# Performance work log

Measured on AMD Instinct MI355X. Metric: run time of the kernel, lower is better.

The kernel has to match this reference:

```python
import jax, jax.numpy as jnp
import numpy as np

B, N, D = 4, 1024, 512
H, Dv, Dq = 8, 64, 64
NUM_BUCKETS = 64
LN_EPS = 1e-5


def setup_inputs() -> dict:
    key = jax.random.key(0)
    ks = jax.random.split(key, 10)
    x = jax.random.normal(ks[0], (B, N, D), dtype=jnp.float32)
    ts = jnp.sort(jax.random.randint(ks[1], (B, N), 0, 1_000_000), axis=1).astype(jnp.int64)
    cm = jnp.triu(jnp.ones((N, N), dtype=bool), k=1)  # causal: mask j > i
    pm = jnp.zeros((B, N), dtype=bool)                # no padding
    uvqk = 0.02 * jax.random.normal(ks[2], (D, 2 * H * Dv + 2 * H * Dq), dtype=jnp.float32)
    lim = float(np.sqrt(6.0 / (H * Dv + D)))
    o_w = jax.random.uniform(ks[3], (H * Dv, D), minval=-lim, maxval=lim, dtype=jnp.float32)
    o_b = jnp.zeros((D,), dtype=jnp.float32)
    ln_x_w = jnp.ones((D,), jnp.float32); ln_x_b = jnp.zeros((D,), jnp.float32)
    ln_a_w = jnp.ones((H * Dv,), jnp.float32); ln_a_b = jnp.zeros((H * Dv,), jnp.float32)
    ts_w = 0.02 * jax.random.normal(ks[4], (NUM_BUCKETS + 1,), dtype=jnp.float32)
    pos_w = 0.02 * jax.random.normal(ks[5], (2 * N - 1,), dtype=jnp.float32)
    return {"x": x, "ts": ts, "cm": cm, "pm": pm, "uvqk": uvqk, "o_w": o_w, "o_b": o_b,
            "ln_x_w": ln_x_w, "ln_x_b": ln_x_b, "ln_a_w": ln_a_w, "ln_a_b": ln_a_b,
            "ts_w": ts_w, "pos_w": pos_w}


def _layernorm(x, w, b):
    m = jnp.mean(x, axis=-1, keepdims=True)
    v = jnp.mean(jnp.square(x - m), axis=-1, keepdims=True)
    return (x - m) / jnp.sqrt(v + LN_EPS) * w + b


def _rel_bias(ts, ts_w, pos_w):
    # positional part: pb[i, j] = pos_w[j - i + N - 1], shape [N, N]
    idx = jnp.arange(N)
    pb = pos_w[idx[None, :] - idx[:, None] + N - 1]
    # bucketed time part
    ext = jnp.concatenate([ts, ts[:, N - 1:N]], axis=1)           # [B, N+1]
    diff = ext[:, 1:, None] - ext[:, None, :-1]                   # [B, N, N]
    logd = jnp.log(jnp.maximum(jnp.abs(diff), 1).astype(jnp.float32))
    bk = jnp.clip((logd / 0.301).astype(jnp.int32), 0, NUM_BUCKETS)
    return pb[None] + ts_w[bk]                                    # [B, N, N]


def reference(x, ts, cm, pm, uvqk, o_w, o_b, ln_x_w, ln_x_b, ln_a_w, ln_a_b, ts_w, pos_w):
    nx = _layernorm(x, ln_x_w, ln_x_b)                            # [B, N, D]
    out = jax.nn.silu(jnp.einsum('bnd,de->bne', nx, uvqk))        # [B, N, 2HDv+2HDq]
    u, v, q, k = jnp.split(out, [H * Dv, 2 * H * Dv, 2 * H * Dv + H * Dq], axis=-1)
    q = q.reshape(B, N, H, Dq)
    k = k.reshape(B, N, H, Dq)
    v = v.reshape(B, N, H, Dv)
    qk = jnp.einsum('bihd,bjhd->bhij', q, k) + _rel_bias(ts, ts_w, pos_w)[:, None]
    qk = jax.nn.silu(qk) / N
    qk = jnp.where(cm[None, None], 0.0, qk)          # causal mask
    qk = jnp.where(pm[:, None, None, :], 0.0, qk)    # padding mask on keys
    ao = jnp.einsum('bhij,bjhd->bihd', qk, v).reshape(B, N, H * Dv)
    ao = _layernorm(ao, ln_a_w, ln_a_b)
    u = u.reshape(B, N, H * Dv)
    y = (u * ao) @ o_w + o_b + x
    return jnp.where(pm[:, :, None], 0.0, y)
```

## Files before the change

kernel.cpp:

```cpp
#include <hip/hip_runtime.h>
#include <hip/hip_bf16.h>


typedef __attribute__((ext_vector_type(8))) short short8;
typedef __attribute__((ext_vector_type(4))) short bf4;
typedef __attribute__((ext_vector_type(4))) float floatx4;

#define MFMA_BF16 __builtin_amdgcn_mfma_f32_16x16x32_bf16

static __device__ __forceinline__ short f2bf(float f) {
  unsigned u = __builtin_bit_cast(unsigned, f);
  u = (u + 0x7fffu + ((u >> 16) & 1u)) >> 16;
  return (short)u;
}
static __device__ __forceinline__ unsigned pk_bf16(float a, float b) {
  __hip_bfloat162 h = __float22bfloat162_rn(float2{a, b});
  unsigned u;
  __builtin_memcpy(&u, &h, 4);
  return u;
}
static __device__ __forceinline__ short lo16(unsigned u) { return (short)(u & 0xffffu); }
static __device__ __forceinline__ short hi16(unsigned u) { return (short)(u >> 16); }
static __device__ __forceinline__ float bf2f(short s) {
  unsigned u = ((unsigned)(unsigned short)s) << 16;
  return __builtin_bit_cast(float, u);
}
static __device__ __forceinline__ float silu_f(float x) {
  return x / (1.f + __expf(-x));
}
static __device__ __forceinline__ void gl_lds16(const void* g, void* l) {
  __builtin_amdgcn_global_load_lds(
      (const __attribute__((address_space(1))) unsigned int*)g,
      (__attribute__((address_space(3))) unsigned int*)l, 16, 0, 0);
}

__global__ __launch_bounds__(256) void prep_kernel(
    const float* __restrict__ x, const int* __restrict__ ts,
    const float* __restrict__ uvqk, const float* __restrict__ o_w,
    const float* __restrict__ ln_x_w, const float* __restrict__ ln_x_b,
    const float* __restrict__ ts_w, const float* __restrict__ pos_w,
    short* __restrict__ nx, short* __restrict__ uvqk_t,
    short* __restrict__ o_wt, short* __restrict__ bias) {
  __shared__ float tile[32][33];
  const int id = blockIdx.x;
  const int t = threadIdx.x;
  if (id < 4096) {
    const int b = id >> 10, i = id & 1023;
    int ie = i + 1; if (ie > 1023) ie = 1023;
    const int tse = ts[(b << 10) + ie];
    const int j0 = t * 4;
    int4 tj = *(const int4*)&ts[(b << 10) + j0];
    const int* tjp = (const int*)&tj;
    float ov[4];
#pragma unroll
    for (int e = 0; e < 4; ++e) {
      int dt = tse - tjp[e];
      float ad = fabsf((float)dt);
      if (ad < 1.f) ad = 1.f;
      int bkt = (int)(__logf(ad) * (1.f / 0.301f));
      if (bkt > 64) bkt = 64;
      ov[e] = pos_w[j0 + e - i + 1023] + ts_w[bkt];
    }
    uint2 o2 = {pk_bf16(ov[0], ov[1]), pk_bf16(ov[2], ov[3])};
    *(uint2*)&bias[((size_t)id << 10) + j0] = o2;
  } else if (id < 5120) {
    const int lane = t & 63;
    const int row = ((id - 4096) << 2) + (t >> 6);
    const int c0 = lane * 8;
    const float* xr = x + (size_t)row * 512;
    float v[8];
    *(float4*)&v[0] = *(const float4*)(xr + c0);
    *(float4*)&v[4] = *(const float4*)(xr + c0 + 4);
    float s = 0.f, sq = 0.f;
#pragma unroll
    for (int e = 0; e < 8; ++e) { s += v[e]; sq += v[e] * v[e]; }
#pragma unroll
    for (int off = 32; off > 0; off >>= 1) {
      s += __shfl_xor(s, off);
      sq += __shfl_xor(sq, off);
    }
    float m = s * (1.f / 512.f);
    float var = sq * (1.f / 512.f) - m * m;
    float rinv = rsqrtf(var + 1e-5f);
    float wv[8], bv[8];
    *(float4*)&wv[0] = *(const float4*)(ln_x_w + c0);
    *(float4*)&wv[4] = *(const float4*)(ln_x_w + c0 + 4);
    *(float4*)&bv[0] = *(const float4*)(ln_x_b + c0);
    *(float4*)&bv[4] = *(const float4*)(ln_x_b + c0 + 4);
    float o[8];
#pragma unroll
    for (int e = 0; e < 8; ++e) o[e] = (v[e] - m) * rinv * wv[e] + bv[e];
    uint4 o4 = {pk_bf16(o[0], o[1]), pk_bf16(o[2], o[3]),
                pk_bf16(o[4], o[5]), pk_bf16(o[6], o[7])};
    *(uint4*)(nx + (size_t)row * 512 + c0) = o4;
  } else {
    const float* src; short* dst; int R, C, bc, br;
    if (id < 6144) {
      int idm = id - 5120;
      src = uvqk; dst = uvqk_t; R = 512; C = 2048;
      bc = (idm & 63) * 32; br = (idm >> 6) * 32;
    } else {
      int idm = id - 6144;
      src = o_w; dst = o_wt; R = 512; C = 512;
      bc = (idm & 15) * 32; br = (idm >> 4) * 32;
    }
    const int c = t & 31, r0 = t >> 5;
#pragma unroll
    for (int p = 0; p < 4; ++p) {
      int r = r0 + p * 8;
      tile[r][c] = src[(size_t)(br + r) * C + bc + c];
    }
    __syncthreads();
#pragma unroll
    for (int p = 0; p < 4; ++p) {
      int r = r0 + p * 8;
      dst[(size_t)(bc + r) * R + br + c] = f2bf(tile[c][r]);
    }
  }
}

__global__ __launch_bounds__(256) void gemm1_kernel(
    const short* __restrict__ A, const short* __restrict__ Bt,
    short* __restrict__ u_buf, short* __restrict__ vt_buf,
    short* __restrict__ q_buf, short* __restrict__ k_buf) {
  __shared__ __align__(16) short As[2][128 * 32];
  __shared__ __align__(16) short Bs[2][128 * 32];
  const int t = threadIdx.x;
  const int lane = t & 63, w = t >> 6;
  const int quad = lane >> 4, l15 = lane & 15;
  const int m0 = blockIdx.x * 128, n0 = blockIdx.y * 128;
  const int wm = (w & 1) * 64, wn = (w >> 1) * 64;
  const int lr = lane >> 2, lc = (lane & 3) * 8;
  floatx4 acc[4][4];
#pragma unroll
  for (int i = 0; i < 4; ++i)
#pragma unroll
    for (int j = 0; j < 4; ++j) acc[i][j] = (floatx4){0.f, 0.f, 0.f, 0.f};

  for (int k0 = 0; k0 < 512; k0 += 64) {
    __syncthreads();
#pragma unroll
    for (int c = 0; c < 2; ++c)
#pragma unroll
      for (int p = 0; p < 2; ++p) {
        int ra = w * 32 + p * 16;
        gl_lds16(&A[(size_t)(m0 + ra + lr) * 512 + k0 + c * 32 + lc], &As[c][ra * 32]);
        gl_lds16(&Bt[(size_t)(n0 + ra + lr) * 512 + k0 + c * 32 + lc], &Bs[c][ra * 32]);
      }
    __syncthreads();
#pragma unroll
    for (int c = 0; c < 2; ++c) {
      short8 af[4], bfr[4];
#pragma unroll
      for (int mi = 0; mi < 4; ++mi) af[mi] = *(const short8*)&As[c][(wm + mi * 16 + l15) * 32 + quad * 8];
#pragma unroll
      for (int ni = 0; ni < 4; ++ni) bfr[ni] = *(const short8*)&Bs[c][(wn + ni * 16 + l15) * 32 + quad * 8];
#pragma unroll
      for (int mi = 0; mi < 4; ++mi)
#pragma unroll
        for (int ni = 0; ni < 4; ++ni)
          acc[mi][ni] = MFMA_BF16(af[mi], bfr[ni], acc[mi][ni], 0, 0, 0);
    }
  }
  const int seg = n0 >> 9, cbase = n0 & 511;
  if (seg == 0) {
#pragma unroll
    for (int mi = 0; mi < 4; ++mi)
#pragma unroll
      for (int ni = 0; ni < 4; ++ni) {
        int row0 = m0 + wm + mi * 16 + quad * 4;
        int c = cbase + wn + ni * 16 + l15;
        float v0 = silu_f(acc[mi][ni][0]), v1 = silu_f(acc[mi][ni][1]);
        float v2 = silu_f(acc[mi][ni][2]), v3 = silu_f(acc[mi][ni][3]);
        unsigned pa = pk_bf16(v0, v1), pb = pk_bf16(v2, v3);
        u_buf[(size_t)row0 * 512 + c] = lo16(pa);
        u_buf[(size_t)(row0 + 1) * 512 + c] = hi16(pa);
        u_buf[(size_t)(row0 + 2) * 512 + c] = lo16(pb);
        u_buf[(size_t)(row0 + 3) * 512 + c] = hi16(pb);
      }
  } else if (seg == 1) {
#pragma unroll
    for (int mi = 0; mi < 4; ++mi)
#pragma unroll
      for (int ni = 0; ni < 4; ++ni) {
        int c = cbase + wn + ni * 16 + l15;
        int h = c >> 6, d = c & 63;
        int row0 = m0 + wm + mi * 16 + quad * 4;
        int b_ = row0 >> 10, nb = row0 & 1023;
        float v0 = silu_f(acc[mi][ni][0]) * (1.f / 1024.f);
        float v1 = silu_f(acc[mi][ni][1]) * (1.f / 1024.f);
        float v2 = silu_f(acc[mi][ni][2]) * (1.f / 1024.f);
        float v3 = silu_f(acc[mi][ni][3]) * (1.f / 1024.f);
        uint2 sv = {pk_bf16(v0, v1), pk_bf16(v2, v3)};
        *(uint2*)&vt_buf[(((size_t)(b_ * 8 + h) * 64 + d) << 10) + nb] = sv;
      }
  } else {
    short* dst = (seg == 2) ? q_buf : k_buf;
#pragma unroll
    for (int mi = 0; mi < 4; ++mi)
#pragma unroll
      for (int ni = 0; ni < 4; ++ni) {
        int row0 = m0 + wm + mi * 16 + quad * 4;
        int c = cbase + wn + ni * 16 + l15;
        int b_ = row0 >> 10, nb = row0 & 1023;
        size_t base = ((((size_t)(b_ * 8 + (c >> 6))) << 10) + nb) * 64 + (c & 63);
        float v0 = silu_f(acc[mi][ni][0]), v1 = silu_f(acc[mi][ni][1]);
        float v2 = silu_f(acc[mi][ni][2]), v3 = silu_f(acc[mi][ni][3]);
        unsigned pa = pk_bf16(v0, v1), pb = pk_bf16(v2, v3);
        dst[base] = lo16(pa);
        dst[base + 64] = hi16(pa);
        dst[base + 128] = lo16(pb);
        dst[base + 192] = hi16(pb);
      }
  }
}

__global__ __launch_bounds__(256, 4) void attn_kernel(
    const short* __restrict__ q_buf, const short* __restrict__ k_buf,
    const short* __restrict__ vt_buf, const short* __restrict__ bias_buf,
    short* __restrict__ ao_part) {
  __shared__ __align__(16) short q_s[64][72];
  __shared__ __align__(16) short k_s[64][72];
  __shared__ __align__(16) short vt_s[64][72];
  __shared__ __align__(16) short p_s[64][72];

  const int t = threadIdx.x;
  const int lane = t & 63, w = t >> 6;
  const int quad = lane >> 4, l15 = lane & 15;
  const int bh = blockIdx.x, pair = blockIdx.y, jh = blockIdx.z;
  const int b = bh >> 3, h = bh & 7;
  const short* qh = q_buf + (size_t)bh * 65536;
  const short* kh = k_buf + (size_t)bh * 65536;
  const short* vth = vt_buf + (size_t)bh * 65536;
  const int sr = t >> 2, sc = (t & 3) * 16;

#pragma unroll
  for (int half = 0; half < 2; ++half) {
    const int it = half ? (15 - pair) : pair;
    const int i0 = it * 64;
    {
      float4 qr0 = *(const float4*)&qh[(size_t)(i0 + sr) * 64 + sc];
      float4 qr1 = *(const float4*)&qh[(size_t)(i0 + sr) * 64 + sc + 8];
      *(float4*)&q_s[sr][sc] = qr0;
      *(float4*)&q_s[sr][sc + 8] = qr1;
    }
    float4 kr0, kr1, vr0, vr1;
    if (jh <= it) {
      int j0 = jh * 64;
      kr0 = *(const float4*)&kh[(size_t)(j0 + sr) * 64 + sc];
      kr1 = *(const float4*)&kh[(size_t)(j0 + sr) * 64 + sc + 8];
      vr0 = *(const float4*)&vth[(size_t)sr * 1024 + j0 + sc];
      vr1 = *(const float4*)&vth[(size_t)sr * 1024 + j0 + sc + 8];
    }
    floatx4 ao0 = {0.f, 0.f, 0.f, 0.f}, ao1 = ao0, ao2 = ao0, ao3 = ao0;
    for (int jt = jh; jt <= it; jt += 4) {
      const int j0 = jt * 64;
      short br[4][4];
      {
        const short* bb = &bias_buf[((size_t)(b * 1024 + i0 + w * 16 + quad * 4) << 10) + j0 + l15];
#pragma unroll
        for (int ni = 0; ni < 4; ++ni)
#pragma unroll
          for (int r2 = 0; r2 < 4; ++r2)
            br[ni][r2] = bb[((size_t)r2 << 10) + ni * 16];
      }
      __syncthreads();
      *(float4*)&k_s[sr][sc] = kr0;
      *(float4*)&k_s[sr][sc + 8] = kr1;
      *(float4*)&vt_s[sr][sc] = vr0;
      *(float4*)&vt_s[sr][sc + 8] = vr1;
      {
        int jn = (jt + 4 <= it) ? jt + 4 : jt;
        int jn0 = jn * 64;
        kr0 = *(const float4*)&kh[(size_t)(jn0 + sr) * 64 + sc];
        kr1 = *(const float4*)&kh[(size_t)(jn0 + sr) * 64 + sc + 8];
        vr0 = *(const float4*)&vth[(size_t)sr * 1024 + jn0 + sc];
        vr1 = *(const float4*)&vth[(size_t)sr * 1024 + jn0 + sc + 8];
      }
      __syncthreads();
      floatx4 s0, s1, s2, s3;
#pragma unroll
      for (int r2 = 0; r2 < 4; ++r2) {
        s0[r2] = bf2f(br[0][r2]);
        s1[r2] = bf2f(br[1][r2]);
        s2[r2] = bf2f(br[2][r2]);
        s3[r2] = bf2f(br[3][r2]);
      }
#pragma unroll
      for (int kk = 0; kk < 64; kk += 32) {
        short8 aq = *(const short8*)&q_s[w * 16 + l15][kk + quad * 8];
        s0 = MFMA_BF16(aq, *(const short8*)&k_s[0 + l15][kk + quad * 8], s0, 0, 0, 0);
        s1 = MFMA_BF16(aq, *(const short8*)&k_s[16 + l15][kk + quad * 8], s1, 0, 0, 0);
        s2 = MFMA_BF16(aq, *(const short8*)&k_s[32 + l15][kk + quad * 8], s2, 0, 0, 0);
        s3 = MFMA_BF16(aq, *(const short8*)&k_s[48 + l15][kk + quad * 8], s3, 0, 0, 0);
      }
      const bool diag = (jt == it);
      floatx4 sv[4] = {s0, s1, s2, s3};
#pragma unroll
      for (int ni = 0; ni < 4; ++ni) {
        int j_loc = ni * 16 + l15;
        float pv[4];
#pragma unroll
        for (int r2 = 0; r2 < 4; ++r2) {
          int i_loc = w * 16 + quad * 4 + r2;
          float p = silu_f(sv[ni][r2]);
          pv[r2] = (diag && j_loc > i_loc) ? 0.f : p;
        }
        unsigned pa = pk_bf16(pv[0], pv[1]), pb = pk_bf16(pv[2], pv[3]);
        int ib = w * 16 + quad * 4;
        p_s[ib][j_loc] = lo16(pa);
        p_s[ib + 1][j_loc] = hi16(pa);
        p_s[ib + 2][j_loc] = lo16(pb);
        p_s[ib + 3][j_loc] = hi16(pb);
      }
#pragma unroll
      for (int kk = 0; kk < 64; kk += 32) {
        short8 ap = *(const short8*)&p_s[w * 16 + l15][kk + quad * 8];
        ao0 = MFMA_BF16(ap, *(const short8*)&vt_s[0 + l15][kk + quad * 8], ao0, 0, 0, 0);
        ao1 = MFMA_BF16(ap, *(const short8*)&vt_s[16 + l15][kk + quad * 8], ao1, 0, 0, 0);
        ao2 = MFMA_BF16(ap, *(const short8*)&vt_s[32 + l15][kk + quad * 8], ao2, 0, 0, 0);
        ao3 = MFMA_BF16(ap, *(const short8*)&vt_s[48 + l15][kk + quad * 8], ao3, 0, 0, 0);
      }
    }
    floatx4 aov[4] = {ao0, ao1, ao2, ao3};
    short* aod = ao_part + (size_t)jh * 2097152;
#pragma unroll
    for (int ni = 0; ni < 4; ++ni) {
      int gi0 = i0 + w * 16 + quad * 4;
      int d = ni * 16 + l15;
      unsigned pa = pk_bf16(aov[ni][0], aov[ni][1]);
      unsigned pb = pk_bf16(aov[ni][2], aov[ni][3]);
      size_t base = ((size_t)(b * 1024 + gi0)) * 512 + h * 64 + d;
      aod[base] = lo16(pa);
      aod[base + 512] = hi16(pa);
      aod[base + 1024] = lo16(pb);
      aod[base + 1536] = hi16(pb);
    }
  }
}

__global__ __launch_bounds__(256) void ln_mul_kernel(
    const short* __restrict__ ao_part, const short* __restrict__ u,
    const float* __restrict__ w_, const float* __restrict__ b_,
    short* __restrict__ g) {
  const int lane = threadIdx.x & 63;
  const int row = (blockIdx.x << 2) + (threadIdx.x >> 6);
  const int c0 = lane * 8;
  short8 a0 = *(const short8*)(ao_part + (size_t)row * 512 + c0);
  short8 a1 = *(const short8*)(ao_part + 2097152 + (size_t)row * 512 + c0);
  short8 a2 = *(const short8*)(ao_part + 4194304 + (size_t)row * 512 + c0);
  short8 a3 = *(const short8*)(ao_part + 6291456 + (size_t)row * 512 + c0);
  float v[8];
#pragma unroll
  for (int e = 0; e < 8; ++e)
    v[e] = (bf2f(a0[e]) + bf2f(a1[e])) + (bf2f(a2[e]) + bf2f(a3[e]));
  float s = 0.f, sq = 0.f;
#pragma unroll
  for (int e = 0; e < 8; ++e) { s += v[e]; sq += v[e] * v[e]; }
#pragma unroll
  for (int off = 32; off > 0; off >>= 1) {
    s += __shfl_xor(s, off);
    sq += __shfl_xor(sq, off);
  }
  float m = s * (1.f / 512.f);
  float var = sq * (1.f / 512.f) - m * m;
  float rinv = rsqrtf(var + 1e-5f);
  float wv[8], bv[8];
  *(float4*)&wv[0] = *(const float4*)(w_ + c0);
  *(float4*)&wv[4] = *(const float4*)(w_ + c0 + 4);
  *(float4*)&bv[0] = *(const float4*)(b_ + c0);
  *(float4*)&bv[4] = *(const float4*)(b_ + c0 + 4);
  short8 uv = *(const short8*)(u + (size_t)row * 512 + c0);
  float o[8];
#pragma unroll
  for (int e = 0; e < 8; ++e)
    o[e] = bf2f(uv[e]) * ((v[e] - m) * rinv * wv[e] + bv[e]);
  uint4 o4 = {pk_bf16(o[0], o[1]), pk_bf16(o[2], o[3]),
              pk_bf16(o[4], o[5]), pk_bf16(o[6], o[7])};
  *(uint4*)(g + (size_t)row * 512 + c0) = o4;
}

__global__ __launch_bounds__(256) void gemm2_kernel(
    const short* __restrict__ G, const short* __restrict__ Wt,
    const float* __restrict__ o_b, const float* __restrict__ x,
    float* __restrict__ out) {
  __shared__ __align__(16) short As[2][64 * 32];
  __shared__ __align__(16) short Bs[2][64 * 32];
  const int t = threadIdx.x;
  const int lane = t & 63, w = t >> 6;
  const int quad = lane >> 4, l15 = lane & 15;
  const int m0 = blockIdx.x * 64, n0 = blockIdx.y * 64;
  const int lr = lane >> 2, lc = (lane & 3) * 8;
  floatx4 acc[4];
#pragma unroll
  for (int j = 0; j < 4; ++j) acc[j] = (floatx4){0.f, 0.f, 0.f, 0.f};

  for (int k0 = 0; k0 < 512; k0 += 64) {
    __syncthreads();
#pragma unroll
    for (int c = 0; c < 2; ++c) {
      int ra = w * 16;
      gl_lds16(&G[(size_t)(m0 + ra + lr) * 512 + k0 + c * 32 + lc], &As[c][ra * 32]);
      gl_lds16(&Wt[(size_t)(n0 + ra + lr) * 512 + k0 + c * 32 + lc], &Bs[c][ra * 32]);
    }
    __syncthreads();
#pragma unroll
    for (int c = 0; c < 2; ++c) {
      short8 af = *(const short8*)&As[c][(w * 16 + l15) * 32 + quad * 8];
#pragma unroll
      for (int ni = 0; ni < 4; ++ni) {
        short8 bfr = *(const short8*)&Bs[c][(ni * 16 + l15) * 32 + quad * 8];
        acc[ni] = MFMA_BF16(af, bfr, acc[ni], 0, 0, 0);
      }
    }
  }
#pragma unroll
  for (int ni = 0; ni < 4; ++ni)
#pragma unroll
    for (int r = 0; r < 4; ++r) {
      int row = m0 + w * 16 + quad * 4 + r;
      int c = n0 + ni * 16 + l15;
      out[(size_t)row * 512 + c] = acc[ni][r] + o_b[c] + x[(size_t)row * 512 + c];
    }
}

extern "C" void kernel_launch(void* const* d_in, const int* in_sizes, int n_in,
                              void* d_out, int out_size, void* d_ws, size_t ws_size,
                              hipStream_t stream) {
  const float* x = (const float*)d_in[0];
  const int* ts = (const int*)d_in[1];
  const float* uvqk = (const float*)d_in[4];
  const float* o_w = (const float*)d_in[5];
  const float* o_b = (const float*)d_in[6];
  const float* ln_x_w = (const float*)d_in[7];
  const float* ln_x_b = (const float*)d_in[8];
  const float* ln_a_w = (const float*)d_in[9];
  const float* ln_a_b = (const float*)d_in[10];
  const float* ts_w = (const float*)d_in[11];
  const float* pos_w = (const float*)d_in[12];
  float* out = (float*)d_out;

  char* ws = (char*)d_ws;
  short* nx = (short*)(ws + 0);
  short* uvqk_t = (short*)(ws + 4194304);
  short* o_wt = (short*)(ws + 6291456);
  short* u_buf = (short*)(ws + 6815744);
  short* q_buf = (short*)(ws + 11010048);
  short* k_buf = (short*)(ws + 15204352);
  short* vt_buf = (short*)(ws + 19398656);
  short* bias_buf = (short*)(ws + 23592960);
  short* ao_part = (short*)(ws + 31981568);
  short* g_buf = nx;

  hipLaunchKernelGGL(prep_kernel, dim3(6400), dim3(256), 0, stream,
                     x, ts, uvqk, o_w, ln_x_w, ln_x_b, ts_w, pos_w,
                     nx, uvqk_t, o_wt, bias_buf);
  hipLaunchKernelGGL(gemm1_kernel, dim3(32, 16), dim3(256), 0, stream, nx, uvqk_t, u_buf, vt_buf, q_buf, k_buf);
  hipLaunchKernelGGL(attn_kernel, dim3(32, 8, 4), dim3(256), 0, stream, q_buf, k_buf, vt_buf, bias_buf, ao_part);
  hipLaunchKernelGGL(ln_mul_kernel, dim3(1024), dim3(256), 0, stream, ao_part, u_buf, ln_a_w, ln_a_b, g_buf);
  hipLaunchKernelGGL(gemm2_kernel, dim3(64, 8), dim3(256), 0, stream, g_buf, o_wt, o_b, x, out);
}
```

Measured before the change: 140.3 us.

## Share K/V tiles across both query tiles in attention; narrow GEMM1 N-tile

The attention kernel now processes its two paired query tiles (pair and 15-pair) inside a single key loop. Each loaded K/V tile is used for both query tiles, and Q fragments stay in registers, which halves K/V global loads and LDS staging and removes the Q shared buffer. Separately, GEMM1 tiles shrink from 128x128 to 128x64 and the grid doubles, giving more blocks to fill the GPU. The cost is more accumulator registers in attention and less per-block reuse of A tiles in GEMM1.

```diff
diff --git a/kernel.cpp b/kernel.cpp
--- a/kernel.cpp
+++ b/kernel.cpp
@@ -124,41 +124,43 @@
     short* __restrict__ u_buf, short* __restrict__ vt_buf,
     short* __restrict__ q_buf, short* __restrict__ k_buf) {
   __shared__ __align__(16) short As[2][128 * 32];
-  __shared__ __align__(16) short Bs[2][128 * 32];
+  __shared__ __align__(16) short Bs[2][64 * 32];
   const int t = threadIdx.x;
   const int lane = t & 63, w = t >> 6;
   const int quad = lane >> 4, l15 = lane & 15;
-  const int m0 = blockIdx.x * 128, n0 = blockIdx.y * 128;
-  const int wm = (w & 1) * 64, wn = (w >> 1) * 64;
+  const int m0 = blockIdx.x * 128, n0 = blockIdx.y * 64;
+  const int wm = (w & 1) * 64, wn = (w >> 1) * 32;
   const int lr = lane >> 2, lc = (lane & 3) * 8;
-  floatx4 acc[4][4];
+  floatx4 acc[4][2];
 #pragma unroll
   for (int i = 0; i < 4; ++i)
 #pragma unroll
-    for (int j = 0; j < 4; ++j) acc[i][j] = (floatx4){0.f, 0.f, 0.f, 0.f};
+    for (int j = 0; j < 2; ++j) acc[i][j] = (floatx4){0.f, 0.f, 0.f, 0.f};
 
   for (int k0 = 0; k0 < 512; k0 += 64) {
     __syncthreads();
 #pragma unroll
-    for (int c = 0; c < 2; ++c)
+    for (int c = 0; c < 2; ++c) {
 #pragma unroll
       for (int p = 0; p < 2; ++p) {
         int ra = w * 32 + p * 16;
         gl_lds16(&A[(size_t)(m0 + ra + lr) * 512 + k0 + c * 32 + lc], &As[c][ra * 32]);
-        gl_lds16(&Bt[(size_t)(n0 + ra + lr) * 512 + k0 + c * 32 + lc], &Bs[c][ra * 32]);
-      }
+      }
+      int rb = w * 16;
+      gl_lds16(&Bt[(size_t)(n0 + rb + lr) * 512 + k0 + c * 32 + lc], &Bs[c][rb * 32]);
+    }
     __syncthreads();
 #pragma unroll
     for (int c = 0; c < 2; ++c) {
-      short8 af[4], bfr[4];
+      short8 af[4], bfr[2];
 #pragma unroll
       for (int mi = 0; mi < 4; ++mi) af[mi] = *(const short8*)&As[c][(wm + mi * 16 + l15) * 32 + quad * 8];
 #pragma unroll
-      for (int ni = 0; ni < 4; ++ni) bfr[ni] = *(const short8*)&Bs[c][(wn + ni * 16 + l15) * 32 + quad * 8];
+      for (int ni = 0; ni < 2; ++ni) bfr[ni] = *(const short8*)&Bs[c][(wn + ni * 16 + l15) * 32 + quad * 8];
 #pragma unroll
       for (int mi = 0; mi < 4; ++mi)
 #pragma unroll
-        for (int ni = 0; ni < 4; ++ni)
+        for (int ni = 0; ni < 2; ++ni)
           acc[mi][ni] = MFMA_BF16(af[mi], bfr[ni], acc[mi][ni], 0, 0, 0);
     }
   }
@@ -167,7 +169,7 @@
 #pragma unroll
     for (int mi = 0; mi < 4; ++mi)
 #pragma unroll
-      for (int ni = 0; ni < 4; ++ni) {
+      for (int ni = 0; ni < 2; ++ni) {
         int row0 = m0 + wm + mi * 16 + quad * 4;
         int c = cbase + wn + ni * 16 + l15;
         float v0 = silu_f(acc[mi][ni][0]), v1 = silu_f(acc[mi][ni][1]);
@@ -182,7 +184,7 @@
 #pragma unroll
     for (int mi = 0; mi < 4; ++mi)
 #pragma unroll
-      for (int ni = 0; ni < 4; ++ni) {
+      for (int ni = 0; ni < 2; ++ni) {
         int c = cbase + wn + ni * 16 + l15;
         int h = c >> 6, d = c & 63;
         int row0 = m0 + wm + mi * 16 + quad * 4;
@@ -199,7 +201,7 @@
 #pragma unroll
     for (int mi = 0; mi < 4; ++mi)
 #pragma unroll
-      for (int ni = 0; ni < 4; ++ni) {
+      for (int ni = 0; ni < 2; ++ni) {
         int row0 = m0 + wm + mi * 16 + quad * 4;
         int c = cbase + wn + ni * 16 + l15;
         int b_ = row0 >> 10, nb = row0 & 1023;
@@ -219,7 +221,6 @@
     const short* __restrict__ q_buf, const short* __restrict__ k_buf,
     const short* __restrict__ vt_buf, const short* __restrict__ bias_buf,
     short* __restrict__ ao_part) {
-  __shared__ __align__(16) short q_s[64][72];
   __shared__ __align__(16) short k_s[64][72];
   __shared__ __align__(16) short vt_s[64][72];
   __shared__ __align__(16) short p_s[64][72];
@@ -233,28 +234,55 @@
   const short* kh = k_buf + (size_t)bh * 65536;
   const short* vth = vt_buf + (size_t)bh * 65536;
   const int sr = t >> 2, sc = (t & 3) * 16;
-
-#pragma unroll
-  for (int half = 0; half < 2; ++half) {
-    const int it = half ? (15 - pair) : pair;
-    const int i0 = it * 64;
+  const int it1 = 15 - pair;
+  const int i0a = pair * 64, i0b = it1 * 64;
+
+  const short* qra = &qh[(size_t)(i0a + w * 16 + l15) * 64 + quad * 8];
+  const short* qrb = &qh[(size_t)(i0b + w * 16 + l15) * 64 + quad * 8];
+  short8 aqa0 = *(const short8*)qra, aqa1 = *(const short8*)(qra + 32);
+  short8 aqb0 = *(const short8*)qrb, aqb1 = *(const short8*)(qrb + 32);
+
+  floatx4 aoa[4], aob[4];
+#pragma unroll
+  for (int ni = 0; ni < 4; ++ni) {
+    aoa[ni] = (floatx4){0.f, 0.f, 0.f, 0.f};
+    aob[ni] = (floatx4){0.f, 0.f, 0.f, 0.f};
+  }
+
+  float4 kr0, kr1, vr0, vr1;
+  {
+    int j0 = jh * 64;
+    kr0 = *(const float4*)&kh[(size_t)(j0 + sr) * 64 + sc];
+    kr1 = *(const float4*)&kh[(size_t)(j0 + sr) * 64 + sc + 8];
+    vr0 = *(const float4*)&vth[(size_t)sr * 1024 + j0 + sc];
+    vr1 = *(const float4*)&vth[(size_t)sr * 1024 + j0 + sc + 8];
+  }
+
+  for (int jt = jh; jt <= it1; jt += 4) {
+    const int j0 = jt * 64;
+    __syncthreads();
+    *(float4*)&k_s[sr][sc] = kr0;
+    *(float4*)&k_s[sr][sc + 8] = kr1;
+    *(float4*)&vt_s[sr][sc] = vr0;
+    *(float4*)&vt_s[sr][sc + 8] = vr1;
     {
-      float4 qr0 = *(const float4*)&qh[(size_t)(i0 + sr) * 64 + sc];
-      float4 qr1 = *(const float4*)&qh[(size_t)(i0 + sr) * 64 + sc + 8];
-      *(float4*)&q_s[sr][sc] = qr0;
-      *(float4*)&q_s[sr][sc + 8] = qr1;
-    }
-    float4 kr0, kr1, vr0, vr1;
-    if (jh <= it) {
-      int j0 = jh * 64;
-      kr0 = *(const float4*)&kh[(size_t)(j0 + sr) * 64 + sc];
-      kr1 = *(const float4*)&kh[(size_t)(j0 + sr) * 64 + sc + 8];
-      vr0 = *(const float4*)&vth[(size_t)sr * 1024 + j0 + sc];
-      vr1 = *(const float4*)&vth[(size_t)sr * 1024 + j0 + sc + 8];
-    }
-    floatx4 ao0 = {0.f, 0.f, 0.f, 0.f}, ao1 = ao0, ao2 = ao0, ao3 = ao0;
-    for (int jt = jh; jt <= it; jt += 4) {
-      const int j0 = jt * 64;
+      int jn = (jt + 4 <= it1) ? jt + 4 : jt;
+      int jn0 = jn * 64;
+      kr0 = *(const float4*)&kh[(size_t)(jn0 + sr) * 64 + sc];
+      kr1 = *(const float4*)&kh[(size_t)(jn0 + sr) * 64 + sc + 8];
+      vr0 = *(const float4*)&vth[(size_t)sr * 1024 + jn0 + sc];
+      vr1 = *(const float4*)&vth[(size_t)sr * 1024 + jn0 + sc + 8];
+    }
+    __syncthreads();
+
+#pragma unroll
+    for (int unit = 0; unit < 2; ++unit) {
+      if (unit == 1 && jt > pair) break;
+      const int i0 = unit ? i0a : i0b;
+      const bool diag = (jt == (unit ? pair : it1));
+      const short8 aq0 = unit ? aqa0 : aqb0;
+      const short8 aq1 = unit ? aqa1 : aqb1;
+      floatx4* ao = unit ? aoa : aob;
       short br[4][4];
       {
         const short* bb = &bias_buf[((size_t)(b * 1024 + i0 + w * 16 + quad * 4) << 10) + j0 + l15];
@@ -264,38 +292,16 @@
           for (int r2 = 0; r2 < 4; ++r2)
             br[ni][r2] = bb[((size_t)r2 << 10) + ni * 16];
       }
-      __syncthreads();
-      *(float4*)&k_s[sr][sc] = kr0;
-      *(float4*)&k_s[sr][sc + 8] = kr1;
-      *(float4*)&vt_s[sr][sc] = vr0;
-      *(float4*)&vt_s[sr][sc + 8] = vr1;
-      {
-        int jn = (jt + 4 <= it) ? jt + 4 : jt;
-        int jn0 = jn * 64;
-        kr0 = *(const float4*)&kh[(size_t)(jn0 + sr) * 64 + sc];
-        kr1 = *(const float4*)&kh[(size_t)(jn0 + sr) * 64 + sc + 8];
-        vr0 = *(const float4*)&vth[(size_t)sr * 1024 + jn0 + sc];
-        vr1 = *(const float4*)&vth[(size_t)sr * 1024 + jn0 + sc + 8];
-      }
-      __syncthreads();
-      floatx4 s0, s1, s2, s3;
-#pragma unroll
-      for (int r2 = 0; r2 < 4; ++r2) {
-        s0[r2] = bf2f(br[0][r2]);
-        s1[r2] = bf2f(br[1][r2]);
-        s2[r2] = bf2f(br[2][r2]);
-        s3[r2] = bf2f(br[3][r2]);
-      }
-#pragma unroll
-      for (int kk = 0; kk < 64; kk += 32) {
-        short8 aq = *(const short8*)&q_s[w * 16 + l15][kk + quad * 8];
-        s0 = MFMA_BF16(aq, *(const short8*)&k_s[0 + l15][kk + quad * 8], s0, 0, 0, 0);
-        s1 = MFMA_BF16(aq, *(const short8*)&k_s[16 + l15][kk + quad * 8], s1, 0, 0, 0);
-        s2 = MFMA_BF16(aq, *(const short8*)&k_s[32 + l15][kk + quad * 8], s2, 0, 0, 0);
-        s3 = MFMA_BF16(aq, *(const short8*)&k_s[48 + l15][kk + quad * 8], s3, 0, 0, 0);
-      }
-      const bool diag = (jt == it);
-      floatx4 sv[4] = {s0, s1, s2, s3};
+      floatx4 s[4];
+#pragma unroll
+      for (int ni = 0; ni < 4; ++ni)
+#pragma unroll
+        for (int r2 = 0; r2 < 4; ++r2) s[ni][r2] = bf2f(br[ni][r2]);
+#pragma unroll
+      for (int ni = 0; ni < 4; ++ni) {
+        s[ni] = MFMA_BF16(aq0, *(const short8*)&k_s[ni * 16 + l15][quad * 8], s[ni], 0, 0, 0);
+        s[ni] = MFMA_BF16(aq1, *(const short8*)&k_s[ni * 16 + l15][32 + quad * 8], s[ni], 0, 0, 0);
+      }
 #pragma unroll
       for (int ni = 0; ni < 4; ++ni) {
         int j_loc = ni * 16 + l15;
@@ -303,7 +309,7 @@
 #pragma unroll
         for (int r2 = 0; r2 < 4; ++r2) {
           int i_loc = w * 16 + quad * 4 + r2;
-          float p = silu_f(sv[ni][r2]);
+          float p = silu_f(s[ni][r2]);
           pv[r2] = (diag && j_loc > i_loc) ? 0.f : p;
         }
         unsigned pa = pk_bf16(pv[0], pv[1]), pb = pk_bf16(pv[2], pv[3]);
@@ -313,23 +319,26 @@
         p_s[ib + 2][j_loc] = lo16(pb);
         p_s[ib + 3][j_loc] = hi16(pb);
       }
-#pragma unroll
-      for (int kk = 0; kk < 64; kk += 32) {
-        short8 ap = *(const short8*)&p_s[w * 16 + l15][kk + quad * 8];
-        ao0 = MFMA_BF16(ap, *(const short8*)&vt_s[0 + l15][kk + quad * 8], ao0, 0, 0, 0);
-        ao1 = MFMA_BF16(ap, *(const short8*)&vt_s[16 + l15][kk + quad * 8], ao1, 0, 0, 0);
-        ao2 = MFMA_BF16(ap, *(const short8*)&vt_s[32 + l15][kk + quad * 8], ao2, 0, 0, 0);
-        ao3 = MFMA_BF16(ap, *(const short8*)&vt_s[48 + l15][kk + quad * 8], ao3, 0, 0, 0);
-      }
-    }
-    floatx4 aov[4] = {ao0, ao1, ao2, ao3};
-    short* aod = ao_part + (size_t)jh * 2097152;
+      short8 ap0 = *(const short8*)&p_s[w * 16 + l15][quad * 8];
+      short8 ap1 = *(const short8*)&p_s[w * 16 + l15][32 + quad * 8];
+#pragma unroll
+      for (int ni = 0; ni < 4; ++ni) {
+        ao[ni] = MFMA_BF16(ap0, *(const short8*)&vt_s[ni * 16 + l15][quad * 8], ao[ni], 0, 0, 0);
+        ao[ni] = MFMA_BF16(ap1, *(const short8*)&vt_s[ni * 16 + l15][32 + quad * 8], ao[ni], 0, 0, 0);
+      }
+    }
+  }
+  short* aod = ao_part + (size_t)jh * 2097152;
+#pragma unroll
+  for (int half = 0; half < 2; ++half) {
+    const int i0 = half ? i0b : i0a;
+    floatx4* ao = half ? aob : aoa;
 #pragma unroll
     for (int ni = 0; ni < 4; ++ni) {
       int gi0 = i0 + w * 16 + quad * 4;
       int d = ni * 16 + l15;
-      unsigned pa = pk_bf16(aov[ni][0], aov[ni][1]);
-      unsigned pb = pk_bf16(aov[ni][2], aov[ni][3]);
+      unsigned pa = pk_bf16(ao[ni][0], ao[ni][1]);
+      unsigned pb = pk_bf16(ao[ni][2], ao[ni][3]);
       size_t base = ((size_t)(b * 1024 + gi0)) * 512 + h * 64 + d;
       aod[base] = lo16(pa);
       aod[base + 512] = hi16(pa);
@@ -455,7 +464,7 @@
   hipLaunchKernelGGL(prep_kernel, dim3(6400), dim3(256), 0, stream,
                      x, ts, uvqk, o_w, ln_x_w, ln_x_b, ts_w, pos_w,
                      nx, uvqk_t, o_wt, bias_buf);
-  hipLaunchKernelGGL(gemm1_kernel, dim3(32, 16), dim3(256), 0, stream, nx, uvqk_t, u_buf, vt_buf, q_buf, k_buf);
+  hipLaunchKernelGGL(gemm1_kernel, dim3(32, 32), dim3(256), 0, stream, nx, uvqk_t, u_buf, vt_buf, q_buf, k_buf);
   hipLaunchKernelGGL(attn_kernel, dim3(32, 8, 4), dim3(256), 0, stream, q_buf, k_buf, vt_buf, bias_buf, ao_part);
   hipLaunchKernelGGL(ln_mul_kernel, dim3(1024), dim3(256), 0, stream, ao_part, u_buf, ln_a_w, ln_a_b, g_buf);
   hipLaunchKernelGGL(gemm2_kernel, dim3(64, 8), dim3(256), 0, stream, g_buf, o_wt, o_b, x, out);
```

After: 141.0 us. About the same (+0.5%).

## Load Q/K/Vt tiles via direct global-to-LDS copies with split-K layout

Applied to the files above, without the earlier changes.

Replaces the register-staged global loads of the Q, K and V^T tiles with direct global-to-LDS copies (gl_lds16) and reorganizes the LDS tiles into two 32-column unpadded halves. This drops the register prefetch of the next K/V tile and the VGPR pressure and LDS store instructions that came with it. The unpadded 32-wide layout may cause LDS bank conflicts on the MFMA operand reads and P writes. Loads are no longer overlapped with the previous iteration's compute, since the copy is issued between the two barriers.

```diff
diff --git a/kernel.cpp b/kernel.cpp
--- a/kernel.cpp
+++ b/kernel.cpp
@@ -3,7 +3,6 @@
 
 
 typedef __attribute__((ext_vector_type(8))) short short8;
-typedef __attribute__((ext_vector_type(4))) short bf4;
 typedef __attribute__((ext_vector_type(4))) float floatx4;
 
 #define MFMA_BF16 __builtin_amdgcn_mfma_f32_16x16x32_bf16
@@ -219,10 +218,10 @@
     const short* __restrict__ q_buf, const short* __restrict__ k_buf,
     const short* __restrict__ vt_buf, const short* __restrict__ bias_buf,
     short* __restrict__ ao_part) {
-  __shared__ __align__(16) short q_s[64][72];
-  __shared__ __align__(16) short k_s[64][72];
-  __shared__ __align__(16) short vt_s[64][72];
-  __shared__ __align__(16) short p_s[64][72];
+  __shared__ __align__(16) short q_s[2][64 * 32];
+  __shared__ __align__(16) short k_s[2][64 * 32];
+  __shared__ __align__(16) short vt_s[2][64 * 32];
+  __shared__ __align__(16) short p_s[2][64 * 32];
 
   const int t = threadIdx.x;
   const int lane = t & 63, w = t >> 6;
@@ -232,26 +231,16 @@
   const short* qh = q_buf + (size_t)bh * 65536;
   const short* kh = k_buf + (size_t)bh * 65536;
   const short* vth = vt_buf + (size_t)bh * 65536;
-  const int sr = t >> 2, sc = (t & 3) * 16;
+  const int glr = lane >> 2;
+  const int glc = (lane & 3) * 8;
 
 #pragma unroll
   for (int half = 0; half < 2; ++half) {
     const int it = half ? (15 - pair) : pair;
     const int i0 = it * 64;
-    {
-      float4 qr0 = *(const float4*)&qh[(size_t)(i0 + sr) * 64 + sc];
-      float4 qr1 = *(const float4*)&qh[(size_t)(i0 + sr) * 64 + sc + 8];
-      *(float4*)&q_s[sr][sc] = qr0;
-      *(float4*)&q_s[sr][sc + 8] = qr1;
-    }
-    float4 kr0, kr1, vr0, vr1;
-    if (jh <= it) {
-      int j0 = jh * 64;
-      kr0 = *(const float4*)&kh[(size_t)(j0 + sr) * 64 + sc];
-      kr1 = *(const float4*)&kh[(size_t)(j0 + sr) * 64 + sc + 8];
-      vr0 = *(const float4*)&vth[(size_t)sr * 1024 + j0 + sc];
-      vr1 = *(const float4*)&vth[(size_t)sr * 1024 + j0 + sc + 8];
-    }
+#pragma unroll
+    for (int c = 0; c < 2; ++c)
+      gl_lds16(&qh[(size_t)(i0 + w * 16 + glr) * 64 + c * 32 + glc], &q_s[c][w * 512]);
     floatx4 ao0 = {0.f, 0.f, 0.f, 0.f}, ao1 = ao0, ao2 = ao0, ao3 = ao0;
     for (int jt = jh; jt <= it; jt += 4) {
       const int j0 = jt * 64;
@@ -265,17 +254,10 @@
             br[ni][r2] = bb[((size_t)r2 << 10) + ni * 16];
       }
       __syncthreads();
-      *(float4*)&k_s[sr][sc] = kr0;
-      *(float4*)&k_s[sr][sc + 8] = kr1;
-      *(float4*)&vt_s[sr][sc] = vr0;
-      *(float4*)&vt_s[sr][sc + 8] = vr1;
-      {
-        int jn = (jt + 4 <= it) ? jt + 4 : jt;
-        int jn0 = jn * 64;
-        kr0 = *(const float4*)&kh[(size_t)(jn0 + sr) * 64 + sc];
-        kr1 = *(const float4*)&kh[(size_t)(jn0 + sr) * 64 + sc + 8];
-        vr0 = *(const float4*)&vth[(size_t)sr * 1024 + jn0 + sc];
-        vr1 = *(const float4*)&vth[(size_t)sr * 1024 + jn0 + sc + 8];
+#pragma unroll
+      for (int c = 0; c < 2; ++c) {
+        gl_lds16(&kh[(size_t)(j0 + w * 16 + glr) * 64 + c * 32 + glc], &k_s[c][w * 512]);
+        gl_lds16(&vth[(size_t)(w * 16 + glr) * 1024 + j0 + c * 32 + glc], &vt_s[c][w * 512]);
       }
       __syncthreads();
       floatx4 s0, s1, s2, s3;
@@ -287,18 +269,19 @@
         s3[r2] = bf2f(br[3][r2]);
       }
 #pragma unroll
-      for (int kk = 0; kk < 64; kk += 32) {
-        short8 aq = *(const short8*)&q_s[w * 16 + l15][kk + quad * 8];
-        s0 = MFMA_BF16(aq, *(const short8*)&k_s[0 + l15][kk + quad * 8], s0, 0, 0, 0);
-        s1 = MFMA_BF16(aq, *(const short8*)&k_s[16 + l15][kk + quad * 8], s1, 0, 0, 0);
-        s2 = MFMA_BF16(aq, *(const short8*)&k_s[32 + l15][kk + quad * 8], s2, 0, 0, 0);
-        s3 = MFMA_BF16(aq, *(const short8*)&k_s[48 + l15][kk + quad * 8], s3, 0, 0, 0);
+      for (int c = 0; c < 2; ++c) {
+        short8 aq = *(const short8*)&q_s[c][(w * 16 + l15) * 32 + quad * 8];
+        s0 = MFMA_BF16(aq, *(const short8*)&k_s[c][(0 + l15) * 32 + quad * 8], s0, 0, 0, 0);
+        s1 = MFMA_BF16(aq, *(const short8*)&k_s[c][(16 + l15) * 32 + quad * 8], s1, 0, 0, 0);
+        s2 = MFMA_BF16(aq, *(const short8*)&k_s[c][(32 + l15) * 32 + quad * 8], s2, 0, 0, 0);
+        s3 = MFMA_BF16(aq, *(const short8*)&k_s[c][(48 + l15) * 32 + quad * 8], s3, 0, 0, 0);
       }
       const bool diag = (jt == it);
       floatx4 sv[4] = {s0, s1, s2, s3};
 #pragma unroll
       for (int ni = 0; ni < 4; ++ni) {
         int j_loc = ni * 16 + l15;
+        int pc = ni >> 1, pcol = (ni & 1) * 16 + l15;
         float pv[4];
 #pragma unroll
         for (int r2 = 0; r2 < 4; ++r2) {
@@ -308,18 +291,18 @@
         }
         unsigned pa = pk_bf16(pv[0], pv[1]), pb = pk_bf16(pv[2], pv[3]);
         int ib = w * 16 + quad * 4;
-        p_s[ib][j_loc] = lo16(pa);
-        p_s[ib + 1][j_loc] = hi16(pa);
-        p_s[ib + 2][j_loc] = lo16(pb);
-        p_s[ib + 3][j_loc] = hi16(pb);
-      }
-#pragma unroll
-      for (int kk = 0; kk < 64; kk += 32) {
-        short8 ap = *(const short8*)&p_s[w * 16 + l15][kk + quad * 8];
-        ao0 = MFMA_BF16(ap, *(const short8*)&vt_s[0 + l15][kk + quad * 8], ao0, 0, 0, 0);
-        ao1 = MFMA_BF16(ap, *(const short8*)&vt_s[16 + l15][kk + quad * 8], ao1, 0, 0, 0);
-        ao2 = MFMA_BF16(ap, *(const short8*)&vt_s[32 + l15][kk + quad * 8], ao2, 0, 0, 0);
-        ao3 = MFMA_BF16(ap, *(const short8*)&vt_s[48 + l15][kk + quad * 8], ao3, 0, 0, 0);
+        p_s[pc][ib * 32 + pcol] = lo16(pa);
+        p_s[pc][(ib + 1) * 32 + pcol] = hi16(pa);
+        p_s[pc][(ib + 2) * 32 + pcol] = lo16(pb);
+        p_s[pc][(ib + 3) * 32 + pcol] = hi16(pb);
+      }
+#pragma unroll
+      for (int c = 0; c < 2; ++c) {
+        short8 ap = *(const short8*)&p_s[c][(w * 16 + l15) * 32 + quad * 8];
+        ao0 = MFMA_BF16(ap, *(const short8*)&vt_s[c][(0 + l15) * 32 + quad * 8], ao0, 0, 0, 0);
+        ao1 = MFMA_BF16(ap, *(const short8*)&vt_s[c][(16 + l15) * 32 + quad * 8], ao1, 0, 0, 0);
+        ao2 = MFMA_BF16(ap, *(const short8*)&vt_s[c][(32 + l15) * 32 + quad * 8], ao2, 0, 0, 0);
+        ao3 = MFMA_BF16(ap, *(const short8*)&vt_s[c][(48 + l15) * 32 + quad * 8], ao3, 0, 0, 0);
       }
     }
     floatx4 aov[4] = {ao0, ao1, ao2, ao3};
```

New measurement: 141.3 us. No clear change (+0.7%).
